# Performance work log

Hardware: AMD Instinct MI355X
Metric: run time of the kernel (lower is better)

Reference implementation:

```python
import jax, jax.numpy as jnp
import numpy as np

N = 50000      # nodes
E = 1200000    # edges
G = 256        # graphs in batch
H = 64         # hidden_dim
F_IN = 5       # input_dim
L = 3          # num deep GCN layers
EPS_BN = 1e-5
EPS_MSG = 1e-7

def setup_inputs() -> dict:
    key = jax.random.key(0)
    ks = jax.random.split(key, 12)
    r = lambda i, shp, s=0.1: jax.random.normal(ks[i], shp, jnp.float32) * s
    return {
        "x": jax.random.normal(ks[0], (N, F_IN), jnp.float32),
        "edge_index": jax.random.randint(ks[1], (2, E), 0, N),
        "batch_idx": jnp.sort(jax.random.randint(ks[2], (N,), 0, G)),
        "conv1_W": r(3, (F_IN, H)), "conv1_b": jnp.zeros((H,), jnp.float32),
        "bn1_g": jnp.ones((H,), jnp.float32), "bn1_b": jnp.zeros((H,), jnp.float32),
        "ln_g": jnp.ones((L, H), jnp.float32), "ln_b": jnp.zeros((L, H), jnp.float32),
        "prelu_a": jnp.full((L, H), 0.25, jnp.float32),
        "gen_t": jnp.ones((L,), jnp.float32),
        "mlp_W1": r(4, (L, H, 2 * H)), "mlp_b1": jnp.zeros((L, 2 * H), jnp.float32),
        "mlp_bn_g": jnp.ones((L, 2 * H), jnp.float32), "mlp_bn_b": jnp.zeros((L, 2 * H), jnp.float32),
        "mlp_W2": r(5, (L, 2 * H, H)), "mlp_b2": jnp.zeros((L, H), jnp.float32),
        "lin1_W": r(6, ((L + 1) * H * 2, 2 * H)), "lin1_b": jnp.zeros((2 * H,), jnp.float32),
        "lin2_W": r(7, (2 * H, H)), "lin2_b": jnp.zeros((H,), jnp.float32),
        "out_W": r(8, (H, 1)), "out_b": jnp.zeros((1,), jnp.float32),
    }

def _layernorm(x, g, b):
    mu = jnp.mean(x, axis=-1, keepdims=True)
    var = jnp.mean(jnp.square(x - mu), axis=-1, keepdims=True)
    return (x - mu) * jax.lax.rsqrt(var + EPS_BN) * g + b

def _prelu(x, a):
    return jnp.where(x >= 0, x, a * x)

def _bn_eval(x, g, b):
    # eval-mode BatchNorm with running_mean=0, running_var=1
    return x * (g / jnp.sqrt(1.0 + EPS_BN)) + b

def reference(x, edge_index, batch_idx, conv1_W, conv1_b, bn1_g, bn1_b,
              ln_g, ln_b, prelu_a, gen_t, mlp_W1, mlp_b1, mlp_bn_g, mlp_bn_b,
              mlp_W2, mlp_b2, lin1_W, lin1_b, lin2_W, lin2_b, out_W, out_b):
    n = x.shape[0]
    src, dst = edge_index[0], edge_index[1]

    # ---- GCNConv (with self loops, symmetric normalization) ----
    loops = jnp.arange(n)
    row = jnp.concatenate([src, loops])  # [E+N]
    col = jnp.concatenate([dst, loops])
    h = x @ conv1_W
    deg = jax.ops.segment_sum(jnp.ones_like(col, jnp.float32), col, num_segments=n)
    dinv = jnp.where(deg > 0, deg ** -0.5, 0.0)
    norm = dinv[row] * dinv[col]
    h = jax.ops.segment_sum(h[row] * norm[:, None], col, num_segments=n) + conv1_b
    h = _bn_eval(h, bn1_g, bn1_b)
    h = jax.nn.relu(h)

    xs = [h]
    # ---- DeepGCNLayer (res+) x L, GENConv with softmax aggregation ----
    for i in range(ln_g.shape[0]):
        u = _layernorm(h, ln_g[i], ln_b[i])
        u = _prelu(u, prelu_a[i])
        msg = jax.nn.relu(u[src]) + EPS_MSG            # [E, H]
        sc = msg * gen_t[i]
        m = jax.ops.segment_max(sc, dst, num_segments=n)
        e = jnp.exp(sc - m[dst])
        s = jax.ops.segment_sum(e, dst, num_segments=n)
        alpha = e / s[dst]                             # segment-wise softmax per channel
        agg = jax.ops.segment_sum(msg * alpha, dst, num_segments=n) + u  # root add
        z = agg @ mlp_W1[i] + mlp_b1[i]
        z = _bn_eval(z, mlp_bn_g[i], mlp_bn_b[i])
        z = jax.nn.relu(z)
        z = z @ mlp_W2[i] + mlp_b2[i]
        h = h + z                                      # res+
        xs.append(h)

    # ---- JumpingKnowledge cat + global mean/max pool ----
    xc = jnp.concatenate(xs, axis=1)                   # [N, 4H]
    cnt = jax.ops.segment_sum(jnp.ones((n,), jnp.float32), batch_idx, num_segments=G)
    xmean = jax.ops.segment_sum(xc, batch_idx, num_segments=G) / jnp.maximum(cnt, 1.0)[:, None]
    xmax = jax.ops.segment_max(xc, batch_idx, num_segments=G)
    xmax = jnp.where(jnp.isfinite(xmax), xmax, 0.0)
    p = jnp.concatenate([xmean, xmax], axis=1)         # [G, 8H]

    # ---- readout MLP (dropout off in eval) ----
    p = jax.nn.relu(p @ lin1_W + lin1_b)
    p = jax.nn.relu(p @ lin2_W + lin2_b)
    return p @ out_W + out_b
```

## Files before the change

kernel.cpp:

```cpp
#include <hip/hip_runtime.h>
#include <math.h>

#define NND 50000
#define NE  1200000
#define NG  256
#define H   64
#define H2  128
#define H4  256
#define H8  512
#define FIN 5
#define EPS_BN 1e-5f
#define EPS_MSG 1e-7f
#define NB 196
#define TILES 196
#define TCAP 7168
#define EPB 4096
#define NB1 293
#define ELLC 72
#define PC 8
#define MT 64

typedef _Float16 half8 __attribute__((ext_vector_type(8)));
typedef _Float16 half4 __attribute__((ext_vector_type(4)));
typedef float floatx4 __attribute__((ext_vector_type(4)));


__global__ void k_setup(const int* __restrict__ batch, int* tilecur, int* __restrict__ gstart,
                        const float* __restrict__ x, float* __restrict__ xp,
                        const float* __restrict__ W1, const float* __restrict__ W2,
                        _Float16* __restrict__ w1f, _Float16* __restrict__ w2f) {
    int b = blockIdx.x, t = threadIdx.x;
    if (b < NB) {
        int n = b * 256 + t;
        if (n < NND) {
            float a0 = x[n * FIN + 0], a1 = x[n * FIN + 1], a2 = x[n * FIN + 2];
            float a3 = x[n * FIN + 3], a4 = x[n * FIN + 4];
            *(float4*)&xp[n * 8] = make_float4(a0, a1, a2, a3);
            *(float4*)&xp[n * 8 + 4] = make_float4(a4, 0.f, 0.f, 0.f);
        }
        return;
    }
    if (b == NB || b == NB + 1) {
        if (b == NB && t < TILES) tilecur[t] = 0;
        int g = (b - NB) * 256 + t;
        if (g > NG) return;
        int lo = 0, hi = NND;
        while (lo < hi) { int mid = (lo + hi) >> 1; if (batch[mid] < g) lo = mid + 1; else hi = mid; }
        gstart[g] = lo;
        return;
    }
    int tt = (b - NB - 2) * 256 + t;
    if (tt >= 3 * 16 * 64) return;
    int lane = tt & 63, fr = (tt >> 6) & 15, l = tt >> 10;
    {
        int jt = fr >> 1, kf = fr & 1;
        int j = jt * 16 + (lane & 15);
        int k0 = kf * 32 + (lane >> 4) * 8;
#pragma unroll
        for (int i = 0; i < 8; i++)
            w1f[(((size_t)l * 16 + jt * 2 + kf) * 64 + lane) * 8 + i] =
                (_Float16)W1[(size_t)l * H * H2 + (k0 + i) * H2 + j];
    }
    {
        int ct = fr >> 2, k2f = fr & 3;
        int c = ct * 16 + (lane & 15);
        int k0 = k2f * 32 + (lane >> 4) * 8;
#pragma unroll
        for (int i = 0; i < 8; i++)
            w2f[(((size_t)l * 16 + ct * 4 + k2f) * 64 + lane) * 8 + i] =
                (_Float16)W2[(size_t)l * H2 * H + (k0 + i) * H + c];
    }
}


__global__ void __launch_bounds__(256)
k_bin1(const int* __restrict__ ei, int* tilecur, unsigned* __restrict__ tilebuf) {
    __shared__ int cnt[TILES];
    __shared__ int base[TILES];
    int b = blockIdx.x, t = threadIdx.x;
    for (int i = t; i < TILES; i += 256) cnt[i] = 0;
    __syncthreads();
    int e0 = b * EPB;
#pragma unroll
    for (int r = 0; r < EPB / 256; r++) {
        int e = e0 + r * 256 + t;
        if (e < NE) atomicAdd(&cnt[ei[NE + e] >> 8], 1);
    }
    __syncthreads();
    for (int i = t; i < TILES; i += 256) {
        base[i] = atomicAdd(&tilecur[i], cnt[i]);
        cnt[i] = 0;
    }
    __syncthreads();
#pragma unroll
    for (int r = 0; r < EPB / 256; r++) {
        int e = e0 + r * 256 + t;
        if (e < NE) {
            int s = ei[e], d = ei[NE + e];
            int tile = d >> 8;
            int pos = base[tile] + atomicAdd(&cnt[tile], 1);
            if (pos < TCAP)
                tilebuf[(size_t)tile * TCAP + pos] = ((unsigned)s << 8) | (unsigned)(d & 255);
        }
    }
}

__global__ void __launch_bounds__(256)
k_bin2(const int* __restrict__ tilecur, const unsigned* __restrict__ tilebuf,
       unsigned short* __restrict__ ell, int* __restrict__ deg, float* __restrict__ dinv) {
    __shared__ unsigned short ell_l[256 * ELLC];
    __shared__ int cnt[256];
    int tile = blockIdx.x, t = threadIdx.x;
    cnt[t] = 0;
    __syncthreads();
    int n = min(tilecur[tile], TCAP);
    for (int i = t; i < n; i += 256) {
        unsigned v = tilebuf[(size_t)tile * TCAP + i];
        int dl = v & 255u;
        int slot = atomicAdd(&cnt[dl], 1);
        if (slot < ELLC) ell_l[dl * ELLC + slot] = (unsigned short)(v >> 8);
    }
    __syncthreads();
    const unsigned* s32 = (const unsigned*)ell_l;
    unsigned* d32 = (unsigned*)(ell + (size_t)tile * 256 * ELLC);
    for (int i = t; i < 256 * ELLC / 2; i += 256) d32[i] = s32[i];
    int d = tile * 256 + t;
    if (d < NND) {
        deg[d] = min(cnt[t], ELLC);
        dinv[d] = rsqrtf((float)cnt[t] + 1.0f);
    }
}


__global__ void k_gcn(const int* __restrict__ deg, const unsigned short* __restrict__ ell,
                      const float* __restrict__ xp, const float* __restrict__ dinv,
                      const float* __restrict__ W,
                      const float* __restrict__ cb, const float* __restrict__ bg,
                      const float* __restrict__ bb,
                      const float* __restrict__ lg, const float* __restrict__ lb,
                      const float* __restrict__ pa,
                      _Float16* __restrict__ xcH, _Float16* __restrict__ u_h) {
    int tid = blockIdx.x * blockDim.x + threadIdx.x;
    int d = tid >> 4;
    int r = threadIdx.x & 15;
    if (d >= NND) return;
    int dg = deg[d];
    size_t base = (size_t)d * ELLC;
    float xw0 = 0.f, xw1 = 0.f, xw2 = 0.f, xw3 = 0.f, xw4 = 0.f;
    for (int i = r; i < dg; i += 16) {
        int s = (int)ell[base + i];
        float dv = dinv[s];
        float4 a = *(const float4*)&xp[s * 8];
        float a4 = xp[s * 8 + 4];
        xw0 += a.x * dv; xw1 += a.y * dv; xw2 += a.z * dv;
        xw3 += a.w * dv; xw4 += a4 * dv;
    }
#pragma unroll
    for (int off = 1; off <= 8; off <<= 1) {
        xw0 += __shfl_xor(xw0, off, 64);
        xw1 += __shfl_xor(xw1, off, 64);
        xw2 += __shfl_xor(xw2, off, 64);
        xw3 += __shfl_xor(xw3, off, 64);
        xw4 += __shfl_xor(xw4, off, 64);
    }
    float dd = dinv[d];
    float4 xa = *(const float4*)&xp[d * 8];
    float xa4 = xp[d * 8 + 4];
    xw0 += dd * xa.x; xw1 += dd * xa.y; xw2 += dd * xa.z;
    xw3 += dd * xa.w; xw4 += dd * xa4;
    float bns = rsqrtf(1.f + EPS_BN);
    float x0[4];
    float sum = 0.f, sq = 0.f;
#pragma unroll
    for (int j = 0; j < 4; j++) {
        int c = 4 * r + j;
        float s_ = xw0 * W[c] + xw1 * W[H + c] + xw2 * W[2 * H + c]
                 + xw3 * W[3 * H + c] + xw4 * W[4 * H + c];
        float v = s_ * dd + cb[c];
        v = v * (bg[c] * bns) + bb[c];
        v = fmaxf(v, 0.f);
        x0[j] = v;
        sum += v; sq += v * v;
    }
    {
        half4 xh = {(_Float16)x0[0], (_Float16)x0[1], (_Float16)x0[2], (_Float16)x0[3]};
        *(half4*)&xcH[(size_t)d * H4 + 4 * r] = xh;
    }
#pragma unroll
    for (int off = 1; off <= 8; off <<= 1) {
        sum += __shfl_xor(sum, off, 64);
        sq  += __shfl_xor(sq,  off, 64);
    }
    float mu  = sum * (1.f / H);
    float var = sq * (1.f / H) - mu * mu;
    float rs = rsqrtf(var + EPS_BN);
    half4 yh;
#pragma unroll
    for (int j = 0; j < 4; j++) {
        int c = 4 * r + j;
        float y = (x0[j] - mu) * rs * lg[c] + lb[c];
        y = (y >= 0.f) ? y : pa[c] * y;
        yh[j] = (_Float16)y;
    }
    *(half4*)&u_h[(size_t)d * H + 4 * r] = yh;
}


__global__ void k_gen(const int* __restrict__ deg, const unsigned short* __restrict__ ell,
                      const _Float16* __restrict__ u_h,
                      const float* __restrict__ tptr, int li, _Float16* __restrict__ ua_h) {
    int d = (blockIdx.x * blockDim.x + threadIdx.x) >> 6;
    int lane = threadIdx.x & 63;
    if (d >= NND) return;
    int q = lane & 15, eg = lane >> 4;
    float t = tptr[li];
    int dg = deg[d];
    size_t base = (size_t)d * ELLC;
    half4 us = *(const half4*)&u_h[(size_t)d * H + 4 * q];
    float4 s4 = {0.f, 0.f, 0.f, 0.f}, n4 = {0.f, 0.f, 0.f, 0.f};
    for (int i0 = 0; i0 < dg; i0 += 64) {
        int idx = i0 + lane;
        int csrv = (idx < dg) ? (int)ell[base + idx] : 0;
        int chunk = min(64, dg - i0);
        for (int j = 0; j < chunk; j += 32) {
            half4 uv[8]; bool ok[8];
#pragma unroll
            for (int b2 = 0; b2 < 8; b2++) {
                int e_rel = j + 4 * b2 + eg;
                int s = __shfl(csrv, e_rel, 64);
                ok[b2] = (e_rel < chunk);
                uv[b2] = (half4){0, 0, 0, 0};
                if (ok[b2]) uv[b2] = *(const half4*)&u_h[(size_t)s * H + 4 * q];
            }
#pragma unroll
            for (int b2 = 0; b2 < 8; b2++) {
                if (ok[b2]) {
                    float m0 = fmaxf((float)uv[b2][0], 0.f) + EPS_MSG;
                    float m1 = fmaxf((float)uv[b2][1], 0.f) + EPS_MSG;
                    float m2 = fmaxf((float)uv[b2][2], 0.f) + EPS_MSG;
                    float m3 = fmaxf((float)uv[b2][3], 0.f) + EPS_MSG;
                    float e0 = __expf(m0 * t - 8.f);
                    float e1 = __expf(m1 * t - 8.f);
                    float e2 = __expf(m2 * t - 8.f);
                    float e3 = __expf(m3 * t - 8.f);
                    s4.x += e0; s4.y += e1; s4.z += e2; s4.w += e3;
                    n4.x += m0 * e0; n4.y += m1 * e1; n4.z += m2 * e2; n4.w += m3 * e3;
                }
            }
        }
    }
#pragma unroll
    for (int off = 16; off <= 32; off <<= 1) {
        s4.x += __shfl_xor(s4.x, off, 64); s4.y += __shfl_xor(s4.y, off, 64);
        s4.z += __shfl_xor(s4.z, off, 64); s4.w += __shfl_xor(s4.w, off, 64);
        n4.x += __shfl_xor(n4.x, off, 64); n4.y += __shfl_xor(n4.y, off, 64);
        n4.z += __shfl_xor(n4.z, off, 64); n4.w += __shfl_xor(n4.w, off, 64);
    }
    if (eg == 0) {
        float o0 = (float)us[0] + ((s4.x > 0.f) ? n4.x / s4.x : 0.f);
        float o1 = (float)us[1] + ((s4.y > 0.f) ? n4.y / s4.y : 0.f);
        float o2 = (float)us[2] + ((s4.z > 0.f) ? n4.z / s4.z : 0.f);
        float o3 = (float)us[3] + ((s4.w > 0.f) ? n4.w / s4.w : 0.f);
        half4 oh = {(_Float16)o0, (_Float16)o1, (_Float16)o2, (_Float16)o3};
        *(half4*)&ua_h[(size_t)d * H + 4 * q] = oh;
    }
}


__global__ void __launch_bounds__(256)
k_mlp(const _Float16* __restrict__ ua_h,
      const _Float16* __restrict__ w1f, const _Float16* __restrict__ w2f,
      const float* __restrict__ b1,
      const float* __restrict__ bng, const float* __restrict__ bnb,
      const float* __restrict__ b2,
      _Float16* __restrict__ xcH, int slice,
      const float* __restrict__ lg, const float* __restrict__ lb,
      const float* __restrict__ pa, _Float16* __restrict__ u_h, int do_ln) {
    __shared__ _Float16 a2[4][4][64][8];
    int t = threadIdx.x;
    int w = t >> 6, l = t & 63;
    int nb = blockIdx.x * MT;
    int c_in = l & 15, quad = l >> 4;
    bool wvalid = (nb + 16 * w) < NND;

    half8 af0 = {0,0,0,0,0,0,0,0}, af1 = af0;
    {
        int node = nb + 16 * w + c_in;
        if (node < NND) {
            af0 = *(const half8*)&u_h[0];
            af0 = *(const half8*)&ua_h[(size_t)node * H + quad * 8];
            af1 = *(const half8*)&ua_h[(size_t)node * H + 32 + quad * 8];
        }
    }

    floatx4 acc[8];
#pragma unroll
    for (int jt = 0; jt < 8; jt++) acc[jt] = (floatx4){0.f, 0.f, 0.f, 0.f};
#pragma unroll
    for (int jt = 0; jt < 8; jt++) {
        half8 bf0 = *(const half8*)&w1f[((size_t)(jt * 2 + 0) * 64 + l) * 8];
        half8 bf1 = *(const half8*)&w1f[((size_t)(jt * 2 + 1) * 64 + l) * 8];
        acc[jt] = __builtin_amdgcn_mfma_f32_16x16x32_f16(af0, bf0, acc[jt], 0, 0, 0);
        acc[jt] = __builtin_amdgcn_mfma_f32_16x16x32_f16(af1, bf1, acc[jt], 0, 0, 0);
    }

    {
        float bns = rsqrtf(1.f + EPS_BN);
#pragma unroll
        for (int jt = 0; jt < 8; jt++) {
            int j = jt * 16 + c_in;
            float b1v = b1[j], bsv = bng[j] * bns, bbv = bnb[j];
            int kf2 = jt >> 1;
            int lp = 16 * ((2 * jt + (c_in >> 3)) & 3);
            int ii = c_in & 7;
#pragma unroll
            for (int reg = 0; reg < 4; reg++) {
                float z = fmaxf((acc[jt][reg] + b1v) * bsv + bbv, 0.f);
                a2[w][kf2][quad * 4 + reg + lp][ii] = (_Float16)z;
            }
        }
    }

    floatx4 acc2[4];
#pragma unroll
    for (int ct = 0; ct < 4; ct++) acc2[ct] = (floatx4){0.f, 0.f, 0.f, 0.f};
    half8 a2f[4];
#pragma unroll
    for (int k2f = 0; k2f < 4; k2f++) a2f[k2f] = *(half8*)&a2[w][k2f][l][0];
#pragma unroll
    for (int ct = 0; ct < 4; ct++) {
#pragma unroll
        for (int k2f = 0; k2f < 4; k2f++) {
            half8 bfr = *(const half8*)&w2f[((size_t)(ct * 4 + k2f) * 64 + l) * 8];
            acc2[ct] = __builtin_amdgcn_mfma_f32_16x16x32_f16(a2f[k2f], bfr, acc2[ct], 0, 0, 0);
        }
    }

    float vv[4][4];
#pragma unroll
    for (int ct = 0; ct < 4; ct++) {
        int c = ct * 16 + c_in;
        float b2v = b2[c];
#pragma unroll
        for (int reg = 0; reg < 4; reg++) {
            int node = nb + 16 * w + quad * 4 + reg;
            float v = 0.f;
            if (wvalid) {
                v = (float)xcH[(size_t)node * H4 + slice * H + c] + acc2[ct][reg] + b2v;
                xcH[(size_t)node * H4 + (slice + 1) * H + c] = (_Float16)v;
            }
            vv[ct][reg] = v;
        }
    }
    if (do_ln) {
#pragma unroll
        for (int reg = 0; reg < 4; reg++) {
            float s = (vv[0][reg] + vv[1][reg]) + (vv[2][reg] + vv[3][reg]);
            float q = (vv[0][reg] * vv[0][reg] + vv[1][reg] * vv[1][reg]) +
                      (vv[2][reg] * vv[2][reg] + vv[3][reg] * vv[3][reg]);
#pragma unroll
            for (int off = 1; off <= 8; off <<= 1) {
                s += __shfl_xor(s, off, 64);
                q += __shfl_xor(q, off, 64);
            }
            float mu = s * (1.f / H);
            float var = q * (1.f / H) - mu * mu;
            float rs = rsqrtf(var + EPS_BN);
            int node = nb + 16 * w + quad * 4 + reg;
#pragma unroll
            for (int ct = 0; ct < 4; ct++) {
                int c = ct * 16 + c_in;
                float y = (vv[ct][reg] - mu) * rs * lg[c] + lb[c];
                y = (y >= 0.f) ? y : pa[c] * y;
                if (wvalid) u_h[(size_t)node * H + c] = (_Float16)y;
            }
        }
    }
}


__global__ void __launch_bounds__(256)
k_pool1(const _Float16* __restrict__ xcH, const int* __restrict__ gstart,
        float* __restrict__ psum_p, float* __restrict__ pmax_p) {
    __shared__ float4 ssum[256];
    __shared__ float4 smax[256];
    int b = blockIdx.x;
    int g = b >> 3, k = b & (PC - 1);
    int t = threadIdx.x;
    int start = gstart[g], end = gstart[g + 1];
    int len = end - start;
    int c0 = start + (len * k) / PC;
    int c1 = start + (len * (k + 1)) / PC;
    int q = t & 63, sub = t >> 6;
    float4 sum = {0.f, 0.f, 0.f, 0.f};
    float4 mx = {-INFINITY, -INFINITY, -INFINITY, -INFINITY};
    for (int n = c0 + sub; n < c1; n += 4) {
        half4 vh = *(const half4*)&xcH[(size_t)n * H4 + 4 * q];
        float v0 = (float)vh[0], v1 = (float)vh[1], v2 = (float)vh[2], v3 = (float)vh[3];
        sum.x += v0; sum.y += v1; sum.z += v2; sum.w += v3;
        mx.x = fmaxf(mx.x, v0); mx.y = fmaxf(mx.y, v1);
        mx.z = fmaxf(mx.z, v2); mx.w = fmaxf(mx.w, v3);
    }
    ssum[t] = sum; smax[t] = mx;
    __syncthreads();
    if (t < 64) {
        float4 s0 = ssum[t], s1 = ssum[t + 64], s2 = ssum[t + 128], s3 = ssum[t + 192];
        float4 m0 = smax[t], m1 = smax[t + 64], m2 = smax[t + 128], m3 = smax[t + 192];
        float4 S, M;
        S.x = (s0.x + s1.x) + (s2.x + s3.x);
        S.y = (s0.y + s1.y) + (s2.y + s3.y);
        S.z = (s0.z + s1.z) + (s2.z + s3.z);
        S.w = (s0.w + s1.w) + (s2.w + s3.w);
        M.x = fmaxf(fmaxf(m0.x, m1.x), fmaxf(m2.x, m3.x));
        M.y = fmaxf(fmaxf(m0.y, m1.y), fmaxf(m2.y, m3.y));
        M.z = fmaxf(fmaxf(m0.z, m1.z), fmaxf(m2.z, m3.z));
        M.w = fmaxf(fmaxf(m0.w, m1.w), fmaxf(m2.w, m3.w));
        *(float4*)&psum_p[(size_t)b * H4 + 4 * q] = S;
        *(float4*)&pmax_p[(size_t)b * H4 + 4 * q] = M;
    }
}

__global__ void __launch_bounds__(256)
k_readout(const float* __restrict__ psum_p, const float* __restrict__ pmax_p,
          const int* __restrict__ gstart,
          const float* __restrict__ W1, const float* __restrict__ b1,
          const float* __restrict__ W2, const float* __restrict__ b2,
          const float* __restrict__ Wo, const float* __restrict__ bo,
          float* __restrict__ out) {
    __shared__ float p0_l[H8];
    __shared__ float p1part[2][H2];
    __shared__ float p1_l[H2];
    __shared__ float p2part[4][H];
    __shared__ float p2_l[H];
    int g = blockIdx.x;
    int t = threadIdx.x;

    {
        float s = 0.f, m = -INFINITY;
#pragma unroll
        for (int k = 0; k < PC; k++) {
            s += psum_p[(size_t)(g * PC + k) * H4 + t];
            m = fmaxf(m, pmax_p[(size_t)(g * PC + k) * H4 + t]);
        }
        int cnt = gstart[g + 1] - gstart[g];
        p0_l[t] = s / fmaxf((float)cnt, 1.f);
        p0_l[H4 + t] = (cnt > 0) ? m : 0.f;
    }
    __syncthreads();

    {
        int j = t & 127, h = t >> 7;
        float acc = 0.f;
        int k0 = h * 256;
        for (int k = 0; k < 256; k++) acc += p0_l[k0 + k] * W1[(k0 + k) * H2 + j];
        p1part[h][j] = acc;
    }
    __syncthreads();
    if (t < H2) p1_l[t] = fmaxf(p1part[0][t] + p1part[1][t] + b1[t], 0.f);
    __syncthreads();

    {
        int c = t & 63, h = t >> 6;
        float acc = 0.f;
        int k0 = h * 32;
        for (int k = 0; k < 32; k++) acc += p1_l[k0 + k] * W2[(k0 + k) * H + c];
        p2part[h][c] = acc;
    }
    __syncthreads();
    if (t < H) p2_l[t] = fmaxf(((p2part[0][t] + p2part[1][t]) + (p2part[2][t] + p2part[3][t])) + b2[t], 0.f);
    __syncthreads();

    if (t < 64) {
        float v = p2_l[t] * Wo[t];
#pragma unroll
        for (int off = 32; off >= 1; off >>= 1) v += __shfl_xor(v, off, 64);
        if (t == 0) out[g] = v + bo[0];
    }
}

extern "C" void kernel_launch(void* const* d_in, const int* in_sizes, int n_in,
                              void* d_out, int out_size, void* d_ws, size_t ws_size,
                              hipStream_t stream) {
    const float* x       = (const float*)d_in[0];
    const int*   ei      = (const int*)d_in[1];
    const int*   batch   = (const int*)d_in[2];
    const float* conv1_W = (const float*)d_in[3];
    const float* conv1_b = (const float*)d_in[4];
    const float* bn1_g   = (const float*)d_in[5];
    const float* bn1_b   = (const float*)d_in[6];
    const float* ln_g    = (const float*)d_in[7];
    const float* ln_b    = (const float*)d_in[8];
    const float* prelu_a = (const float*)d_in[9];
    const float* gen_t   = (const float*)d_in[10];
    const float* mlp_W1  = (const float*)d_in[11];
    const float* mlp_b1  = (const float*)d_in[12];
    const float* mlp_bng = (const float*)d_in[13];
    const float* mlp_bnb = (const float*)d_in[14];
    const float* mlp_W2  = (const float*)d_in[15];
    const float* mlp_b2  = (const float*)d_in[16];
    const float* lin1_W  = (const float*)d_in[17];
    const float* lin1_b  = (const float*)d_in[18];
    const float* lin2_W  = (const float*)d_in[19];
    const float* lin2_b  = (const float*)d_in[20];
    const float* out_W   = (const float*)d_in[21];
    const float* out_b   = (const float*)d_in[22];
    float* out = (float*)d_out;

    float* ws   = (float*)d_ws;
    _Float16* xcH = (_Float16*)ws;
    float* xp   = (float*)(xcH + (size_t)NND * H4);
    float* dinv = xp + (size_t)NND * 8;
    int* deg    = (int*)(dinv + NND);
    int* gstart = deg + NND;
    int* tilecur = gstart + NG + 1;
    unsigned* tilebuf = (unsigned*)(tilecur + TILES);
    unsigned short* ell = (unsigned short*)(tilebuf + (size_t)TILES * TCAP);
    uintptr_t wb = (uintptr_t)(ell + (size_t)TILES * 256 * ELLC);
    wb = (wb + 15) & ~(uintptr_t)15;
    _Float16* w1f = (_Float16*)wb;
    _Float16* w2f = w1f + 3 * 8192;
    _Float16* u_h  = w2f + 3 * 8192;
    _Float16* ua_h = u_h + (size_t)NND * H;
    uintptr_t pb = (uintptr_t)(ua_h + (size_t)NND * H);
    pb = (pb + 15) & ~(uintptr_t)15;
    float* psum_p = (float*)pb;
    float* pmax_p = psum_p + (size_t)NG * PC * H4;

    const int B = 256;
    const int gGCN = (NND * 16 + B - 1) / B;
    const int gNH  = (NND * H) / B;
    const int gMLP = (NND + MT - 1) / MT;

    k_setup<<<NB + 2 + 12, B, 0, stream>>>(batch, tilecur, gstart, x, xp,
                                           mlp_W1, mlp_W2, w1f, w2f);
    k_bin1<<<NB1, B, 0, stream>>>(ei, tilecur, tilebuf);
    k_bin2<<<TILES, B, 0, stream>>>(tilecur, tilebuf, ell, deg, dinv);

    k_gcn<<<gGCN, B, 0, stream>>>(deg, ell, xp, dinv, conv1_W, conv1_b, bn1_g, bn1_b,
                                  ln_g, ln_b, prelu_a, xcH, u_h);

    for (int i = 0; i < 3; i++) {
        k_gen<<<gNH, B, 0, stream>>>(deg, ell, u_h, gen_t, i, ua_h);
        int do_ln = (i < 2) ? 1 : 0;
        k_mlp<<<gMLP, B, 0, stream>>>(ua_h,
                                      w1f + (size_t)i * 8192, w2f + (size_t)i * 8192,
                                      mlp_b1 + i * H2,
                                      mlp_bng + i * H2, mlp_bnb + i * H2,
                                      mlp_b2 + i * H,
                                      xcH, i,
                                      ln_g + (i + 1) * H, ln_b + (i + 1) * H,
                                      prelu_a + (i + 1) * H, u_h, do_ln);
    }

    k_pool1<<<NG * PC, B, 0, stream>>>(xcH, gstart, psum_p, pmax_p);
    k_readout<<<NG, B, 0, stream>>>(psum_p, pmax_p, gstart,
                                    lin1_W, lin1_b, lin2_W, lin2_b, out_W, out_b, out);
}
```

Before: 329.7 us.

## Merge edge binning into setup kernel, pack dinv into xp, add nontemporal accesses

Folds the first edge-binning pass into the setup kernel, replacing one launch with a memset, so binning runs alongside the feature packing and weight conversion. The per-node normalization factor is stored in the padding slot of the packed feature array, so the GCN gather fetches features and dinv with one row read instead of a separate random load. Many global loads and stores (tile buffer, ELL, xcH) become nontemporal to reduce cache pollution. It also drops a redundant load in the MLP kernel. Nontemporal hints may hurt where data is reused soon, for example ELL read three times by k_gen.

```diff
diff --git a/kernel.cpp b/kernel.cpp
--- a/kernel.cpp
+++ b/kernel.cpp
@@ -16,6 +16,7 @@
 #define TCAP 7168
 #define EPB 4096
 #define NB1 293
+#define MRG (NB + 14)
 #define ELLC 72
 #define PC 8
 #define MT 64
@@ -25,11 +26,45 @@
 typedef float floatx4 __attribute__((ext_vector_type(4)));
 
 
-__global__ void k_setup(const int* __restrict__ batch, int* tilecur, int* __restrict__ gstart,
-                        const float* __restrict__ x, float* __restrict__ xp,
-                        const float* __restrict__ W1, const float* __restrict__ W2,
-                        _Float16* __restrict__ w1f, _Float16* __restrict__ w2f) {
+__global__ void __launch_bounds__(256)
+k_setup(const int* __restrict__ batch, int* tilecur, int* __restrict__ gstart,
+        const float* __restrict__ x, float* __restrict__ xp,
+        const float* __restrict__ W1, const float* __restrict__ W2,
+        _Float16* __restrict__ w1f, _Float16* __restrict__ w2f,
+        const int* __restrict__ ei, unsigned* __restrict__ tilebuf) {
+    __shared__ int cnt[TILES];
+    __shared__ int base[TILES];
     int b = blockIdx.x, t = threadIdx.x;
+    if (b >= MRG) {
+        int bb = b - MRG;
+        for (int i = t; i < TILES; i += 256) cnt[i] = 0;
+        __syncthreads();
+        int e0 = bb * EPB;
+#pragma unroll
+        for (int r = 0; r < EPB / 256; r++) {
+            int e = e0 + r * 256 + t;
+            if (e < NE) atomicAdd(&cnt[ei[NE + e] >> 8], 1);
+        }
+        __syncthreads();
+        for (int i = t; i < TILES; i += 256) {
+            base[i] = atomicAdd(&tilecur[i], cnt[i]);
+            cnt[i] = 0;
+        }
+        __syncthreads();
+#pragma unroll
+        for (int r = 0; r < EPB / 256; r++) {
+            int e = e0 + r * 256 + t;
+            if (e < NE) {
+                int s = ei[e], d = ei[NE + e];
+                int tile = d >> 8;
+                int pos = base[tile] + atomicAdd(&cnt[tile], 1);
+                if (pos < TCAP)
+                    __builtin_nontemporal_store(((unsigned)s << 8) | (unsigned)(d & 255),
+                                                &tilebuf[(size_t)tile * TCAP + pos]);
+            }
+        }
+        return;
+    }
     if (b < NB) {
         int n = b * 256 + t;
         if (n < NND) {
@@ -41,7 +76,6 @@
         return;
     }
     if (b == NB || b == NB + 1) {
-        if (b == NB && t < TILES) tilecur[t] = 0;
         int g = (b - NB) * 256 + t;
         if (g > NG) return;
         int lo = 0, hi = NND;
@@ -74,40 +108,8 @@
 
 
 __global__ void __launch_bounds__(256)
-k_bin1(const int* __restrict__ ei, int* tilecur, unsigned* __restrict__ tilebuf) {
-    __shared__ int cnt[TILES];
-    __shared__ int base[TILES];
-    int b = blockIdx.x, t = threadIdx.x;
-    for (int i = t; i < TILES; i += 256) cnt[i] = 0;
-    __syncthreads();
-    int e0 = b * EPB;
-#pragma unroll
-    for (int r = 0; r < EPB / 256; r++) {
-        int e = e0 + r * 256 + t;
-        if (e < NE) atomicAdd(&cnt[ei[NE + e] >> 8], 1);
-    }
-    __syncthreads();
-    for (int i = t; i < TILES; i += 256) {
-        base[i] = atomicAdd(&tilecur[i], cnt[i]);
-        cnt[i] = 0;
-    }
-    __syncthreads();
-#pragma unroll
-    for (int r = 0; r < EPB / 256; r++) {
-        int e = e0 + r * 256 + t;
-        if (e < NE) {
-            int s = ei[e], d = ei[NE + e];
-            int tile = d >> 8;
-            int pos = base[tile] + atomicAdd(&cnt[tile], 1);
-            if (pos < TCAP)
-                tilebuf[(size_t)tile * TCAP + pos] = ((unsigned)s << 8) | (unsigned)(d & 255);
-        }
-    }
-}
-
-__global__ void __launch_bounds__(256)
 k_bin2(const int* __restrict__ tilecur, const unsigned* __restrict__ tilebuf,
-       unsigned short* __restrict__ ell, int* __restrict__ deg, float* __restrict__ dinv) {
+       unsigned short* __restrict__ ell, int* __restrict__ deg, float* __restrict__ xp) {
     __shared__ unsigned short ell_l[256 * ELLC];
     __shared__ int cnt[256];
     int tile = blockIdx.x, t = threadIdx.x;
@@ -115,7 +117,7 @@
     __syncthreads();
     int n = min(tilecur[tile], TCAP);
     for (int i = t; i < n; i += 256) {
-        unsigned v = tilebuf[(size_t)tile * TCAP + i];
+        unsigned v = __builtin_nontemporal_load(&tilebuf[(size_t)tile * TCAP + i]);
         int dl = v & 255u;
         int slot = atomicAdd(&cnt[dl], 1);
         if (slot < ELLC) ell_l[dl * ELLC + slot] = (unsigned short)(v >> 8);
@@ -123,17 +125,18 @@
     __syncthreads();
     const unsigned* s32 = (const unsigned*)ell_l;
     unsigned* d32 = (unsigned*)(ell + (size_t)tile * 256 * ELLC);
-    for (int i = t; i < 256 * ELLC / 2; i += 256) d32[i] = s32[i];
+    for (int i = t; i < 256 * ELLC / 2; i += 256)
+        __builtin_nontemporal_store(s32[i], &d32[i]);
     int d = tile * 256 + t;
     if (d < NND) {
         deg[d] = min(cnt[t], ELLC);
-        dinv[d] = rsqrtf((float)cnt[t] + 1.0f);
+        xp[(size_t)d * 8 + 5] = rsqrtf((float)cnt[t] + 1.0f);
     }
 }
 
 
 __global__ void k_gcn(const int* __restrict__ deg, const unsigned short* __restrict__ ell,
-                      const float* __restrict__ xp, const float* __restrict__ dinv,
+                      const float* __restrict__ xp,
                       const float* __restrict__ W,
                       const float* __restrict__ cb, const float* __restrict__ bg,
                       const float* __restrict__ bb,
@@ -148,12 +151,12 @@
     size_t base = (size_t)d * ELLC;
     float xw0 = 0.f, xw1 = 0.f, xw2 = 0.f, xw3 = 0.f, xw4 = 0.f;
     for (int i = r; i < dg; i += 16) {
-        int s = (int)ell[base + i];
-        float dv = dinv[s];
+        int s = (int)__builtin_nontemporal_load(&ell[base + i]);
         float4 a = *(const float4*)&xp[s * 8];
-        float a4 = xp[s * 8 + 4];
+        float2 a45 = *(const float2*)&xp[s * 8 + 4];
+        float dv = a45.y;
         xw0 += a.x * dv; xw1 += a.y * dv; xw2 += a.z * dv;
-        xw3 += a.w * dv; xw4 += a4 * dv;
+        xw3 += a.w * dv; xw4 += a45.x * dv;
     }
 #pragma unroll
     for (int off = 1; off <= 8; off <<= 1) {
@@ -163,11 +166,11 @@
         xw3 += __shfl_xor(xw3, off, 64);
         xw4 += __shfl_xor(xw4, off, 64);
     }
-    float dd = dinv[d];
     float4 xa = *(const float4*)&xp[d * 8];
-    float xa4 = xp[d * 8 + 4];
+    float2 xa45 = *(const float2*)&xp[d * 8 + 4];
+    float dd = xa45.y;
     xw0 += dd * xa.x; xw1 += dd * xa.y; xw2 += dd * xa.z;
-    xw3 += dd * xa.w; xw4 += dd * xa4;
+    xw3 += dd * xa.w; xw4 += dd * xa45.x;
     float bns = rsqrtf(1.f + EPS_BN);
     float x0[4];
     float sum = 0.f, sq = 0.f;
@@ -184,7 +187,7 @@
     }
     {
         half4 xh = {(_Float16)x0[0], (_Float16)x0[1], (_Float16)x0[2], (_Float16)x0[3]};
-        *(half4*)&xcH[(size_t)d * H4 + 4 * r] = xh;
+        __builtin_nontemporal_store(xh, (half4*)&xcH[(size_t)d * H4 + 4 * r]);
     }
 #pragma unroll
     for (int off = 1; off <= 8; off <<= 1) {
@@ -220,7 +223,7 @@
     float4 s4 = {0.f, 0.f, 0.f, 0.f}, n4 = {0.f, 0.f, 0.f, 0.f};
     for (int i0 = 0; i0 < dg; i0 += 64) {
         int idx = i0 + lane;
-        int csrv = (idx < dg) ? (int)ell[base + idx] : 0;
+        int csrv = (idx < dg) ? (int)__builtin_nontemporal_load(&ell[base + idx]) : 0;
         int chunk = min(64, dg - i0);
         for (int j = 0; j < chunk; j += 32) {
             half4 uv[8]; bool ok[8];
@@ -287,7 +290,6 @@
     {
         int node = nb + 16 * w + c_in;
         if (node < NND) {
-            af0 = *(const half8*)&u_h[0];
             af0 = *(const half8*)&ua_h[(size_t)node * H + quad * 8];
             af1 = *(const half8*)&ua_h[(size_t)node * H + 32 + quad * 8];
         }
@@ -346,8 +348,9 @@
             int node = nb + 16 * w + quad * 4 + reg;
             float v = 0.f;
             if (wvalid) {
-                v = (float)xcH[(size_t)node * H4 + slice * H + c] + acc2[ct][reg] + b2v;
-                xcH[(size_t)node * H4 + (slice + 1) * H + c] = (_Float16)v;
+                _Float16 prev = __builtin_nontemporal_load(&xcH[(size_t)node * H4 + slice * H + c]);
+                v = (float)prev + acc2[ct][reg] + b2v;
+                __builtin_nontemporal_store((_Float16)v, &xcH[(size_t)node * H4 + (slice + 1) * H + c]);
             }
             vv[ct][reg] = v;
         }
@@ -395,7 +398,7 @@
     float4 sum = {0.f, 0.f, 0.f, 0.f};
     float4 mx = {-INFINITY, -INFINITY, -INFINITY, -INFINITY};
     for (int n = c0 + sub; n < c1; n += 4) {
-        half4 vh = *(const half4*)&xcH[(size_t)n * H4 + 4 * q];
+        half4 vh = __builtin_nontemporal_load((const half4*)&xcH[(size_t)n * H4 + 4 * q]);
         float v0 = (float)vh[0], v1 = (float)vh[1], v2 = (float)vh[2], v3 = (float)vh[3];
         sum.x += v0; sum.y += v1; sum.z += v2; sum.w += v3;
         mx.x = fmaxf(mx.x, v0); mx.y = fmaxf(mx.y, v1);
@@ -509,8 +512,7 @@
     float* ws   = (float*)d_ws;
     _Float16* xcH = (_Float16*)ws;
     float* xp   = (float*)(xcH + (size_t)NND * H4);
-    float* dinv = xp + (size_t)NND * 8;
-    int* deg    = (int*)(dinv + NND);
+    int* deg    = (int*)(xp + (size_t)NND * 8);
     int* gstart = deg + NND;
     int* tilecur = gstart + NG + 1;
     unsigned* tilebuf = (unsigned*)(tilecur + TILES);
@@ -531,12 +533,12 @@
     const int gNH  = (NND * H) / B;
     const int gMLP = (NND + MT - 1) / MT;
 
-    k_setup<<<NB + 2 + 12, B, 0, stream>>>(batch, tilecur, gstart, x, xp,
-                                           mlp_W1, mlp_W2, w1f, w2f);
-    k_bin1<<<NB1, B, 0, stream>>>(ei, tilecur, tilebuf);
-    k_bin2<<<TILES, B, 0, stream>>>(tilecur, tilebuf, ell, deg, dinv);
-
-    k_gcn<<<gGCN, B, 0, stream>>>(deg, ell, xp, dinv, conv1_W, conv1_b, bn1_g, bn1_b,
+    hipMemsetAsync(tilecur, 0, TILES * sizeof(int), stream);
+    k_setup<<<MRG + NB1, B, 0, stream>>>(batch, tilecur, gstart, x, xp,
+                                         mlp_W1, mlp_W2, w1f, w2f, ei, tilebuf);
+    k_bin2<<<TILES, B, 0, stream>>>(tilecur, tilebuf, ell, deg, xp);
+
+    k_gcn<<<gGCN, B, 0, stream>>>(deg, ell, xp, conv1_W, conv1_b, bn1_g, bn1_b,
                                   ln_g, ln_b, prelu_a, xcH, u_h);
 
     for (int i = 0; i < 3; i++) {
```

Result: slower. 382.7 us (+16.1%).
